# Optimization experiments

Measured on AMD Instinct MI355X. Metric: run time of the kernel, lower is better.

## Reference

```python
import jax, jax.numpy as jnp
import numpy as np

B, T, H, NH, HD = 2, 2048, 2048, 16, 128


def setup_inputs() -> dict:
    key = jax.random.key(0)
    k1, k2, k3 = jax.random.split(key, 3)
    hidden_states = jax.random.normal(k1, (B, T, H), dtype=jnp.float32)
    w_qkv = jax.random.normal(k2, (3 * H, H), dtype=jnp.float32) * (1.0 / np.sqrt(H))
    w_out = jax.random.normal(k3, (H, H), dtype=jnp.float32) * (1.0 / np.sqrt(H))
    return {"hidden_states": hidden_states, "w_qkv": w_qkv, "w_out": w_out}


def reference(hidden_states, w_qkv, w_out):
    scale = 1.0 / np.sqrt(HD)
    # qkv projection: torch Linear is x @ W.T with W [out, in]
    qkv = jnp.einsum('bth,oh->bto', hidden_states, w_qkv)  # [B, T, 3H]
    q, k, v = jnp.split(qkv, 3, axis=2)
    # [B, NH, T, HD]
    q = q.reshape(B, T, NH, HD).transpose(0, 2, 1, 3)
    k = k.reshape(B, T, NH, HD).transpose(0, 2, 1, 3)
    v = v.reshape(B, T, NH, HD).transpose(0, 2, 1, 3)
    scores = jnp.einsum('bhqd,bhkd->bhqk', q, k) * scale  # [B, NH, T, T]
    mask = jnp.tril(jnp.ones((T, T), dtype=bool))  # causal
    scores = jnp.where(mask[None, None], scores, -jnp.inf)
    probs = jax.nn.softmax(scores, axis=-1)
    attn = jnp.einsum('bhqk,bhkd->bhqd', probs, v)  # [B, NH, T, HD]
    attn = attn.transpose(0, 2, 1, 3).reshape(B, T, H)
    out = jnp.einsum('bth,oh->bto', attn, w_out)
    return out
```

## Files before the change

kernel.cpp:

```cpp
#include <hip/hip_runtime.h>
#include <cstdint>
#include <cstddef>

typedef _Float16 f16x8 __attribute__((ext_vector_type(8)));
typedef _Float16 f16x4 __attribute__((ext_vector_type(4)));
typedef float    f32x4 __attribute__((ext_vector_type(4)));
typedef unsigned short ushort_t;

#define LOG2E 1.4426950408889634f

constexpr int BATCH = 2;
constexpr int TSEQ  = 2048;
constexpr int HID   = 2048;
constexpr int NH    = 16;
constexpr int HD    = 128;
constexpr int GK    = 2048;
constexpr int NKT   = GK / 64;

__device__ inline f32x4 mfma16(f16x8 a, f16x8 b, f32x4 c) {
    return __builtin_amdgcn_mfma_f32_16x16x32_f16(a, b, c, 0, 0, 0);
}

__device__ inline void async_copy16(const void* src, void* dst_lds) {
    __builtin_amdgcn_global_load_lds(
        (const __attribute__((address_space(1))) uint32_t*)src,
        (__attribute__((address_space(3))) uint32_t*)dst_lds, 16, 0, 0);
}

__global__ __launch_bounds__(256)
void cast_f32_f16(const float4* __restrict__ in, f16x4* __restrict__ out, int n4) {
    int i = blockIdx.x * 256 + threadIdx.x;
    if (i >= n4) return;
    float4 v = in[i];
    f16x4 o = { (_Float16)v.x, (_Float16)v.y, (_Float16)v.z, (_Float16)v.w };
    out[i] = o;
}

template <int MODE>
__global__ __launch_bounds__(512, 2)
void gemm_bt(const _Float16* __restrict__ A, const _Float16* __restrict__ B,
             float* __restrict__ C, _Float16* __restrict__ Qo,
             _Float16* __restrict__ Ko, _Float16* __restrict__ Vo, int NB) {
    __shared__ __align__(16) _Float16 As[3][256 * 64];
    __shared__ __align__(16) _Float16 Bs[3][128 * 64];

    const int tid  = threadIdx.x;
    const int lane = tid & 63;
    const int w    = tid >> 6;
    const int l15  = lane & 15;
    const int lq   = lane >> 4;
    const int wr   = w >> 1, wc = w & 1;

    const int bid = (int)blockIdx.x;
    const int cpx = (int)gridDim.x >> 3;
    const int swz = (bid & 7) * cpx + (bid >> 3);
    const int bn  = swz % NB, bm = swz / NB;
    const int m0  = bm * 256, n0 = bn * 128;

    const _Float16* Ab = A + (size_t)m0 * GK;
    const _Float16* Bb = B + (size_t)n0 * GK;

    auto stage = [&](int t, int b) {
        const int k0 = t * 64;
        #pragma unroll
        for (int it = 0; it < 4; ++it) {
            const int slot = it * 512 + tid;
            const int row = slot >> 3, c16 = slot & 7;
            const int srcb = c16 ^ (row & 7);
            async_copy16(Ab + (size_t)row * GK + k0 + srcb * 8,
                         (char*)As[b] + slot * 16);
        }
        #pragma unroll
        for (int it = 0; it < 2; ++it) {
            const int slot = it * 512 + tid;
            const int row = slot >> 3, c16 = slot & 7;
            const int srcb = c16 ^ (row & 7);
            async_copy16(Bb + (size_t)row * GK + k0 + srcb * 8,
                         (char*)Bs[b] + slot * 16);
        }
    };

    f32x4 acc[4][4] = {};

    stage(0, 0);
    stage(1, 1);

    for (int t = 0; t < NKT; ++t) {
        if (t + 1 < NKT) asm volatile("s_waitcnt vmcnt(6)" ::: "memory");
        else             asm volatile("s_waitcnt vmcnt(0)" ::: "memory");
        __builtin_amdgcn_s_barrier();
        __builtin_amdgcn_sched_barrier(0);

        const char* At_ = (const char*)As[t % 3];
        const char* Bt_ = (const char*)Bs[t % 3];

        f16x8 af[4][2], bff[4][2];
        #pragma unroll
        for (int i = 0; i < 4; ++i)
            #pragma unroll
            for (int kk = 0; kk < 2; ++kk) {
                const int ra = wr * 64 + i * 16 + l15;
                af[i][kk]  = *(const f16x8*)(At_ + ra * 128 + (((kk * 4 + lq) ^ (ra & 7)) << 4));
                const int rb = wc * 64 + i * 16 + l15;
                bff[i][kk] = *(const f16x8*)(Bt_ + rb * 128 + (((kk * 4 + lq) ^ (rb & 7)) << 4));
            }

        if (t + 2 < NKT) stage(t + 2, (t + 2) % 3);

        __builtin_amdgcn_s_setprio(1);
        #pragma unroll
        for (int kk = 0; kk < 2; ++kk)
            #pragma unroll
            for (int i = 0; i < 4; ++i)
                #pragma unroll
                for (int j = 0; j < 4; ++j)
                    acc[i][j] = mfma16(af[i][kk], bff[j][kk], acc[i][j]);
        __builtin_amdgcn_s_setprio(0);
    }

    if (MODE == 0) {
        #pragma unroll
        for (int j = 0; j < 4; ++j) {
            const int ncol = n0 + wc * 64 + j * 16 + l15;
            const int which = ncol >> 11;
            const int oo = ncol & 2047;
            const int head = oo >> 7;
            const int d = oo & 127;
            _Float16* dst = (which == 0) ? Qo : (which == 1) ? Ko : Vo;
            const float scl = (which == 0) ? 0.08838834764831845f : 1.0f;
            #pragma unroll
            for (int i = 0; i < 4; ++i) {
                #pragma unroll
                for (int r = 0; r < 4; ++r) {
                    const int m = m0 + wr * 64 + i * 16 + lq * 4 + r;
                    const int b = m >> 11, tt = m & 2047;
                    dst[((size_t)(b * NH + head) * TSEQ + tt) * HD + d] =
                        (_Float16)(acc[i][j][r] * scl);
                }
            }
        }
    } else {
        #pragma unroll
        for (int i = 0; i < 4; ++i)
            #pragma unroll
            for (int j = 0; j < 4; ++j)
                #pragma unroll
                for (int r = 0; r < 4; ++r) {
                    const int m = m0 + wr * 64 + i * 16 + lq * 4 + r;
                    const int n = n0 + wc * 64 + j * 16 + l15;
                    C[(size_t)m * HID + n] = acc[i][j][r];
                }
    }
}

__global__ __launch_bounds__(256)
void attn_fwd(const _Float16* __restrict__ Q, const _Float16* __restrict__ K,
              const _Float16* __restrict__ V, _Float16* __restrict__ O) {
    __shared__ __align__(16) char Ks[64 * 256];
    __shared__ __align__(16) char Vt[128 * 128];
    __shared__ __align__(16) char Ps[4][2048];

    const int tid  = threadIdx.x;
    const int lane = tid & 63;
    const int w    = tid >> 6;
    const int l15  = lane & 15;
    const int lq   = lane >> 4;

    const int bh   = (int)blockIdx.x & 31;
    const int pair = (int)blockIdx.x >> 5;
    const int b = bh >> 4, h = bh & 15;

    const size_t base = (size_t)bh * TSEQ * HD;
    const _Float16* Qp = Q + base;
    const _Float16* Kp = K + base;
    const _Float16* Vp = V + base;

    const f16x8 ones = { (_Float16)1.f, (_Float16)1.f, (_Float16)1.f, (_Float16)1.f,
                         (_Float16)1.f, (_Float16)1.f, (_Float16)1.f, (_Float16)1.f };

    uint4 vv[4];
    auto loadV = [&](int t) {
        const int row = tid & 63;
        #pragma unroll
        for (int it = 0; it < 4; ++it) {
            const int c8 = w * 4 + it;
            vv[it] = *(const uint4*)(Vp + (size_t)(t * 64 + row) * HD + c8 * 8);
        }
    };
    auto stageK = [&](int t) {
        #pragma unroll
        for (int it = 0; it < 4; ++it) {
            const int slot = it * 256 + tid;
            const int row = slot >> 4, c16 = slot & 15;
            const int srcb = c16 ^ (row & 7);
            async_copy16(Kp + (size_t)(t * 64 + row) * HD + srcb * 8, Ks + slot * 16);
        }
    };
    auto writeV = [&]() {
        const int row = tid & 63;
        #pragma unroll
        for (int it = 0; it < 4; ++it) {
            const int c8 = w * 4 + it;
            const uint32_t wrd[4] = {vv[it].x, vv[it].y, vv[it].z, vv[it].w};
            #pragma unroll
            for (int p2 = 0; p2 < 4; ++p2) {
                const int d0 = c8 * 8 + p2 * 2, d1 = d0 + 1;
                int b0 = d0 * 128 + row * 2; b0 ^= (d0 & 7) << 4;
                int b1 = d1 * 128 + row * 2; b1 ^= (d1 & 7) << 4;
                *(ushort_t*)(Vt + b0) = (ushort_t)(wrd[p2] & 0xffffu);
                *(ushort_t*)(Vt + b1) = (ushort_t)(wrd[p2] >> 16);
            }
        }
    };

    char* Pb = Ps[w];

    for (int phase = 0; phase < 2; ++phase) {
        const int qt = phase ? pair : (31 - pair);
        const int q0 = qt * 64;
        const int NT = qt + 1;

        if (phase) __syncthreads();

        const int qrow = q0 + w * 16 + l15;
        f16x8 qf[4];
        #pragma unroll
        for (int ks = 0; ks < 4; ++ks)
            qf[ks] = *(const f16x8*)(Qp + (size_t)qrow * HD + ks * 32 + lq * 8);

        f32x4 o[8] = {};
        f32x4 osum = {};
        float m_run[4];
        #pragma unroll
        for (int r = 0; r < 4; ++r) m_run[r] = -1e30f;

        stageK(0);
        loadV(0);

        for (int t = 0; t < NT; ++t) {
            writeV();
            __syncthreads();
            if (t + 1 < NT) loadV(t + 1);

            const int kv0 = t * 64;
            f32x4 s[4] = {};
            __builtin_amdgcn_s_setprio(1);
            #pragma unroll
            for (int ks = 0; ks < 4; ++ks) {
                #pragma unroll
                for (int nf = 0; nf < 4; ++nf) {
                    const int r   = nf * 16 + l15;
                    const int blk = (ks * 4 + lq) ^ (r & 7);
                    const f16x8 kf = *(const f16x8*)(Ks + r * 256 + blk * 16);
                    s[nf] = mfma16(qf[ks], kf, s[nf]);
                }
            }
            __builtin_amdgcn_s_setprio(0);

            if (kv0 + 63 > q0 + w * 16) {
                #pragma unroll
                for (int nf = 0; nf < 4; ++nf) {
                    const int kvp = kv0 + nf * 16 + l15;
                    #pragma unroll
                    for (int r = 0; r < 4; ++r)
                        if (kvp > q0 + w * 16 + lq * 4 + r) s[nf][r] = -1e30f;
                }
            }

            bool need = false;
            #pragma unroll
            for (int r = 0; r < 4; ++r) {
                const float v = fmaxf(fmaxf(s[0][r], s[1][r]), fmaxf(s[2][r], s[3][r]));
                need = need || (v > m_run[r] + 5.0f);
            }
            if (__any(need)) {
                float alpha[4];
                #pragma unroll
                for (int r = 0; r < 4; ++r) {
                    float v = fmaxf(fmaxf(s[0][r], s[1][r]), fmaxf(s[2][r], s[3][r]));
                    v = fmaxf(v, __shfl_xor(v, 1));
                    v = fmaxf(v, __shfl_xor(v, 2));
                    v = fmaxf(v, __shfl_xor(v, 4));
                    v = fmaxf(v, __shfl_xor(v, 8));
                    const float mn = fmaxf(m_run[r], v);
                    alpha[r] = __builtin_exp2f((m_run[r] - mn) * LOG2E);
                    m_run[r] = mn;
                }
                #pragma unroll
                for (int df = 0; df < 8; ++df)
                    #pragma unroll
                    for (int r = 0; r < 4; ++r)
                        o[df][r] *= alpha[r];
                #pragma unroll
                for (int r = 0; r < 4; ++r) osum[r] *= alpha[r];
            }

            #pragma unroll
            for (int nf = 0; nf < 4; ++nf) {
                #pragma unroll
                for (int r = 0; r < 4; ++r) {
                    const float p = __builtin_exp2f((s[nf][r] - m_run[r]) * LOG2E);
                    const int qp = lq * 4 + r;
                    int byt = qp * 128 + (nf * 16 + l15) * 2;
                    byt ^= (qp & 7) << 4;
                    union { _Float16 hf; ushort_t u; } cv;
                    cv.hf = (_Float16)p;
                    *(ushort_t*)(Pb + byt) = cv.u;
                }
            }

            __builtin_amdgcn_s_setprio(1);
            #pragma unroll
            for (int ks2 = 0; ks2 < 2; ++ks2) {
                const int pblk = (ks2 * 4 + lq) ^ (l15 & 7);
                const f16x8 pf = *(const f16x8*)(Pb + l15 * 128 + pblk * 16);
                #pragma unroll
                for (int df = 0; df < 8; ++df) {
                    const int vr   = df * 16 + l15;
                    const int vblk = (ks2 * 4 + lq) ^ (vr & 7);
                    const f16x8 vf = *(const f16x8*)(Vt + vr * 128 + vblk * 16);
                    o[df] = mfma16(pf, vf, o[df]);
                }
                osum = mfma16(pf, ones, osum);
            }
            __builtin_amdgcn_s_setprio(0);

            if (t + 1 < NT) {
                __syncthreads();
                stageK(t + 1);
            }
        }

        float rl[4];
        #pragma unroll
        for (int r = 0; r < 4; ++r) rl[r] = 1.0f / osum[r];
        #pragma unroll
        for (int df = 0; df < 8; ++df) {
            #pragma unroll
            for (int r = 0; r < 4; ++r) {
                const int qg = q0 + w * 16 + lq * 4 + r;
                const int dg = df * 16 + l15;
                O[((size_t)(b * TSEQ + qg)) * HID + h * HD + dg] =
                    (_Float16)(o[df][r] * rl[r]);
            }
        }
    }
}

extern "C" void kernel_launch(void* const* d_in, const int* in_sizes, int n_in,
                              void* d_out, int out_size, void* d_ws, size_t ws_size,
                              hipStream_t stream) {
    (void)in_sizes; (void)n_in; (void)out_size; (void)ws_size;
    const float* hs   = (const float*)d_in[0];
    const float* wqkv = (const float*)d_in[1];
    const float* wout = (const float*)d_in[2];

    char* ws = (char*)d_ws;
    size_t off = 0;
    _Float16* hs_h   = (_Float16*)(ws + off); off += (size_t)BATCH * TSEQ * HID * 2;
    _Float16* wqkv_h = (_Float16*)(ws + off); off += (size_t)3 * HID * HID * 2;
    _Float16* wout_h = (_Float16*)(ws + off); off += (size_t)HID * HID * 2;
    _Float16* Qh     = (_Float16*)(ws + off); off += (size_t)BATCH * NH * TSEQ * HD * 2;
    _Float16* Kh     = (_Float16*)(ws + off); off += (size_t)BATCH * NH * TSEQ * HD * 2;
    _Float16* Vh     = (_Float16*)(ws + off); off += (size_t)BATCH * NH * TSEQ * HD * 2;
    _Float16* At     = (_Float16*)(ws + off); off += (size_t)BATCH * TSEQ * HID * 2;

    const int n4_hs   = BATCH * TSEQ * HID / 4;
    const int n4_wqkv = 3 * HID * HID / 4;
    const int n4_wout = HID * HID / 4;
    cast_f32_f16<<<dim3((n4_hs   + 255) / 256), dim3(256), 0, stream>>>((const float4*)hs,   (f16x4*)hs_h,   n4_hs);
    cast_f32_f16<<<dim3((n4_wqkv + 255) / 256), dim3(256), 0, stream>>>((const float4*)wqkv, (f16x4*)wqkv_h, n4_wqkv);
    cast_f32_f16<<<dim3((n4_wout + 255) / 256), dim3(256), 0, stream>>>((const float4*)wout, (f16x4*)wout_h, n4_wout);

    gemm_bt<0><<<dim3(768), dim3(512), 0, stream>>>(
        hs_h, wqkv_h, nullptr, Qh, Kh, Vh, 48);

    attn_fwd<<<dim3(512), dim3(256), 0, stream>>>(Qh, Kh, Vh, At);

    gemm_bt<1><<<dim3(256), dim3(512), 0, stream>>>(
        At, wout_h, (float*)d_out, nullptr, nullptr, nullptr, 16);
}
```

Measured before the change: 267.0 us.

## Shrink GEMM tile to 128x128 with double buffering and merge cast kernels

Reduces the GEMM block tile from 256x128 with 512 threads and triple-buffered LDS to 128x128 with 256 threads and double buffering. An extra barrier after the fragment loads makes it safe to overwrite the current buffer, and the grids double to keep the work covered. The three f32-to-f16 cast launches are merged into one kernel that branches on index range, removing two launches. The smaller tile gives more blocks and a smaller LDS footprint per block, at the cost of lower data reuse per tile and an extra synchronization in each k-iteration.

```diff
diff --git a/kernel.cpp b/kernel.cpp
--- a/kernel.cpp
+++ b/kernel.cpp
@@ -28,21 +28,28 @@
 }
 
 __global__ __launch_bounds__(256)
-void cast_f32_f16(const float4* __restrict__ in, f16x4* __restrict__ out, int n4) {
+void cast_all(const float4* __restrict__ hs, const float4* __restrict__ wqkv,
+              const float4* __restrict__ wout, f16x4* __restrict__ hs_h,
+              f16x4* __restrict__ wqkv_h, f16x4* __restrict__ wout_h,
+              int n_hs, int n_wqkv, int n_wout) {
     int i = blockIdx.x * 256 + threadIdx.x;
-    if (i >= n4) return;
-    float4 v = in[i];
+    const float4* src; f16x4* dst; int j;
+    if (i < n_hs)                 { src = hs;   dst = hs_h;   j = i; }
+    else if (i < n_hs + n_wqkv)   { src = wqkv; dst = wqkv_h; j = i - n_hs; }
+    else if (i < n_hs + n_wqkv + n_wout) { src = wout; dst = wout_h; j = i - n_hs - n_wqkv; }
+    else return;
+    float4 v = src[j];
     f16x4 o = { (_Float16)v.x, (_Float16)v.y, (_Float16)v.z, (_Float16)v.w };
-    out[i] = o;
+    dst[j] = o;
 }
 
 template <int MODE>
-__global__ __launch_bounds__(512, 2)
+__global__ __launch_bounds__(256, 2)
 void gemm_bt(const _Float16* __restrict__ A, const _Float16* __restrict__ B,
              float* __restrict__ C, _Float16* __restrict__ Qo,
              _Float16* __restrict__ Ko, _Float16* __restrict__ Vo, int NB) {
-    __shared__ __align__(16) _Float16 As[3][256 * 64];
-    __shared__ __align__(16) _Float16 Bs[3][128 * 64];
+    __shared__ __align__(16) _Float16 As[2][128 * 64];
+    __shared__ __align__(16) _Float16 Bs[2][128 * 64];
 
     const int tid  = threadIdx.x;
     const int lane = tid & 63;
@@ -55,7 +62,7 @@
     const int cpx = (int)gridDim.x >> 3;
     const int swz = (bid & 7) * cpx + (bid >> 3);
     const int bn  = swz % NB, bm = swz / NB;
-    const int m0  = bm * 256, n0 = bn * 128;
+    const int m0  = bm * 128, n0 = bn * 128;
 
     const _Float16* Ab = A + (size_t)m0 * GK;
     const _Float16* Bb = B + (size_t)n0 * GK;
@@ -64,15 +71,15 @@
         const int k0 = t * 64;
         #pragma unroll
         for (int it = 0; it < 4; ++it) {
-            const int slot = it * 512 + tid;
+            const int slot = it * 256 + tid;
             const int row = slot >> 3, c16 = slot & 7;
             const int srcb = c16 ^ (row & 7);
             async_copy16(Ab + (size_t)row * GK + k0 + srcb * 8,
                          (char*)As[b] + slot * 16);
         }
         #pragma unroll
-        for (int it = 0; it < 2; ++it) {
-            const int slot = it * 512 + tid;
+        for (int it = 0; it < 4; ++it) {
+            const int slot = it * 256 + tid;
             const int row = slot >> 3, c16 = slot & 7;
             const int srcb = c16 ^ (row & 7);
             async_copy16(Bb + (size_t)row * GK + k0 + srcb * 8,
@@ -86,13 +93,14 @@
     stage(1, 1);
 
     for (int t = 0; t < NKT; ++t) {
-        if (t + 1 < NKT) asm volatile("s_waitcnt vmcnt(6)" ::: "memory");
+        const int cur = t & 1;
+        if (t + 1 < NKT) asm volatile("s_waitcnt vmcnt(8)" ::: "memory");
         else             asm volatile("s_waitcnt vmcnt(0)" ::: "memory");
         __builtin_amdgcn_s_barrier();
         __builtin_amdgcn_sched_barrier(0);
 
-        const char* At_ = (const char*)As[t % 3];
-        const char* Bt_ = (const char*)Bs[t % 3];
+        const char* At_ = (const char*)As[cur];
+        const char* Bt_ = (const char*)Bs[cur];
 
         f16x8 af[4][2], bff[4][2];
         #pragma unroll
@@ -104,8 +112,12 @@
                 const int rb = wc * 64 + i * 16 + l15;
                 bff[i][kk] = *(const f16x8*)(Bt_ + rb * 128 + (((kk * 4 + lq) ^ (rb & 7)) << 4));
             }
-
-        if (t + 2 < NKT) stage(t + 2, (t + 2) % 3);
+        asm volatile("s_waitcnt lgkmcnt(0)" ::: "memory");
+        __builtin_amdgcn_sched_barrier(0);
+        __builtin_amdgcn_s_barrier();
+        __builtin_amdgcn_sched_barrier(0);
+
+        if (t + 2 < NKT) stage(t + 2, cur);
 
         __builtin_amdgcn_s_setprio(1);
         #pragma unroll
@@ -368,15 +380,16 @@
     const int n4_hs   = BATCH * TSEQ * HID / 4;
     const int n4_wqkv = 3 * HID * HID / 4;
     const int n4_wout = HID * HID / 4;
-    cast_f32_f16<<<dim3((n4_hs   + 255) / 256), dim3(256), 0, stream>>>((const float4*)hs,   (f16x4*)hs_h,   n4_hs);
-    cast_f32_f16<<<dim3((n4_wqkv + 255) / 256), dim3(256), 0, stream>>>((const float4*)wqkv, (f16x4*)wqkv_h, n4_wqkv);
-    cast_f32_f16<<<dim3((n4_wout + 255) / 256), dim3(256), 0, stream>>>((const float4*)wout, (f16x4*)wout_h, n4_wout);
-
-    gemm_bt<0><<<dim3(768), dim3(512), 0, stream>>>(
+    const int n4_all  = n4_hs + n4_wqkv + n4_wout;
+    cast_all<<<dim3((n4_all + 255) / 256), dim3(256), 0, stream>>>(
+        (const float4*)hs, (const float4*)wqkv, (const float4*)wout,
+        (f16x4*)hs_h, (f16x4*)wqkv_h, (f16x4*)wout_h, n4_hs, n4_wqkv, n4_wout);
+
+    gemm_bt<0><<<dim3(1536), dim3(256), 0, stream>>>(
         hs_h, wqkv_h, nullptr, Qh, Kh, Vh, 48);
 
     attn_fwd<<<dim3(512), dim3(256), 0, stream>>>(Qh, Kh, Vh, At);
 
-    gemm_bt<1><<<dim3(256), dim3(512), 0, stream>>>(
+    gemm_bt<1><<<dim3(512), dim3(256), 0, stream>>>(
         At, wout_h, (float*)d_out, nullptr, nullptr, nullptr, 16);
 }
```

New measurement: 265.8 us. About the same (-0.5%).
